# Kernel tuning notes

Hardware: AMD Instinct MI355X
Metric: run time of the kernel (lower is better)

## Reference

```python
import jax, jax.numpy as jnp
import numpy as np

B, C, H, W_IMG = 4, 4, 512, 512
OUT_CH = 256
POS_NUM = 512
NEG_NUM = 512
M_MARGIN = 0.5
TAU = 0.1
EPS = 1e-8


def setup_inputs() -> dict:
    key = jax.random.key(0)
    k1, k2, k3, k4, k5, k6 = jax.random.split(key, 6)
    d1_fegc = jax.random.normal(k1, (B, C, H, W_IMG), dtype=jnp.float32)
    p_fegc = jax.random.uniform(k2, (B, 1, H, W_IMG), dtype=jnp.float32)
    p_pre = jax.random.uniform(k3, (B, 3, H, W_IMG), dtype=jnp.float32)
    gt = (jax.random.uniform(k4, (B, 1, H, W_IMG)) < 0.5).astype(jnp.float32)
    # parameters of the nn.Linear(in_channel, out_channel)
    W = jax.random.normal(k5, (OUT_CH, C), dtype=jnp.float32) / np.sqrt(C)
    b_fc = jax.random.normal(k6, (OUT_CH,), dtype=jnp.float32) * 0.01
    return {"d1_fegc": d1_fegc, "p_fegc": p_fegc, "p_pre": p_pre, "gt": gt, "W": W, "b_fc": b_fc}


def _sample_idx(mask_flat, key, n):
    # randomized fixed-size sampling of n indices where mask is True
    # (replaces torch.nonzero + randperm with a jit-friendly top-k over random scores)
    score = jnp.where(mask_flat, jax.random.uniform(key, mask_flat.shape), -jnp.inf)
    _, idx = jax.lax.top_k(score, n)
    return idx


def reference(d1_fegc, p_fegc, p_pre, gt, W, b_fc):
    b, c, h, w = d1_fegc.shape
    P = POS_NUM * b
    N = NEG_NUM * b
    # p_overlap channel 3: fegc foreground AND pre argmax-class 0
    fegc_fg = p_fegc[:, 0] >= 0.5                       # [b,h,w]
    pre_cls0 = jnp.argmax(p_pre, axis=1) == 0           # [b,h,w]
    pre_region = fegc_fg & pre_cls0                     # [b,h,w]
    gt_fg = gt[:, 0] > 0.5                              # [b,h,w]
    pos_mask = (pre_region & gt_fg).reshape(-1)         # [b*h*w]
    neg_mask = (pre_region & ~gt_fg).reshape(-1)        # [b*h*w]
    # per-pixel feature vectors from d1_fegc
    feats = d1_fegc.transpose(0, 2, 3, 1).reshape(-1, c)  # [b*h*w, c]
    skey = jax.random.key(42)
    kp, kn = jax.random.split(skey)
    pos_idx = _sample_idx(pos_mask, kp, P)
    neg_idx = _sample_idx(neg_mask, kn, N)
    pts = jnp.concatenate([feats[pos_idx], feats[neg_idx]], axis=0)  # [P+N, c]
    proj = pts @ W.T + b_fc                                           # [P+N, out]
    # F.cosine_similarity with eps=1e-8 norm clamping
    norm = jnp.maximum(jnp.linalg.norm(proj, axis=-1, keepdims=True), EPS)
    normed = proj / norm
    cos_sim = normed @ normed.T                                       # [P+N, P+N]
    T = P + N
    label = jnp.ones((T, T), dtype=cos_sim.dtype)
    label = label.at[:P, P:].set(0.0).at[P:, :P].set(0.0)
    s = cos_sim / TAU
    lam = (1.0 - label) * jnp.square(s) + label * jnp.square(jnp.maximum(M_MARGIN - s, 0.0))
    lam = lam * (1.0 - jnp.eye(T, dtype=lam.dtype))                   # mask self pairs
    denom = jnp.sum(lam != 0).astype(lam.dtype)
    return jnp.sum(lam) / denom
```

## Files before the change

kernel.cpp:

```cpp
#include <hip/hip_runtime.h>
#include <stdint.h>

#define HW       262144u
#define NPIX     1048576u
#define NSEL     2048u
#define NSEG     1024u
#define SEGCAP   16u
#define DENSECAP 3584u

#define OFF_SEG   0u
#define OFF_IDX   262144u
#define OFF_VA    278528u
#define OFF_WA    360448u
#define OFF_PSUM  442368u
#define OFF_PNNZ  446464u
#define OFF_G     450560u

#define TF_ROUND(r) { x0 += x1; x1 = (x1 << (r)) | (x1 >> (32 - (r))); x1 ^= x0; }
__host__ __device__ inline void threefry2x32_(uint32_t k0, uint32_t k1,
                                              uint32_t& x0, uint32_t& x1) {
  uint32_t k2 = k0 ^ k1 ^ 0x1BD11BDAu;
  x0 += k0; x1 += k1;
  TF_ROUND(13) TF_ROUND(15) TF_ROUND(26) TF_ROUND(6)
  x0 += k1; x1 += k2 + 1u;
  TF_ROUND(17) TF_ROUND(29) TF_ROUND(16) TF_ROUND(24)
  x0 += k2; x1 += k0 + 2u;
  TF_ROUND(13) TF_ROUND(15) TF_ROUND(26) TF_ROUND(6)
  x0 += k0; x1 += k1 + 3u;
  TF_ROUND(17) TF_ROUND(29) TF_ROUND(16) TF_ROUND(24)
  x0 += k1; x1 += k2 + 4u;
  TF_ROUND(13) TF_ROUND(15) TF_ROUND(26) TF_ROUND(6)
  x0 += k2; x1 += k0 + 5u;
}

__global__ __launch_bounds__(256) void k_front(
    const float* __restrict__ pfegc, const float* __restrict__ ppre,
    const float* __restrict__ gt, const float* __restrict__ Wm,
    const float* __restrict__ bfc,
    uint32_t kp0, uint32_t kp1, uint32_t kn0, uint32_t kn1,
    uint64_t* __restrict__ seg, float* __restrict__ Gout) {
  __shared__ uint32_t cnt2[2];
  __shared__ float sGw[4][25];
  int t = threadIdx.x;
  uint32_t b = blockIdx.x;
  if (t < 2) cnt2[t] = 0;
  if (t < 2 * (int)SEGCAP) {
    uint32_t list = (uint32_t)t / SEGCAP, slot = (uint32_t)t % SEGCAP;
    seg[((size_t)list * NSEG + b) * SEGCAP + slot] = 0ull;
  }
  __syncthreads();
  uint32_t base = b * 1024u + (uint32_t)t * 4u;
  float4 pf = *(const float4*)(pfegc + base);
  float pfa[4] = { pf.x, pf.y, pf.z, pf.w };
  bool any = (pf.x >= 0.5f) || (pf.y >= 0.5f) || (pf.z >= 0.5f) || (pf.w >= 0.5f);
  if (any) {
    uint32_t hw = base & (HW - 1u);
    uint32_t bb = base >> 18;
    const float* pp = ppre + (size_t)bb * 3u * HW + hw;
    float4 p0 = *(const float4*)pp;
    float4 p1 = *(const float4*)(pp + HW);
    float4 p2 = *(const float4*)(pp + 2u * HW);
    float4 g4 = *(const float4*)(gt + base);
    float p0a[4] = { p0.x, p0.y, p0.z, p0.w };
    float p1a[4] = { p1.x, p1.y, p1.z, p1.w };
    float p2a[4] = { p2.x, p2.y, p2.z, p2.w };
    float ga[4]  = { g4.x, g4.y, g4.z, g4.w };
    #pragma unroll
    for (int j = 0; j < 4; ++j) {
      if (pfa[j] >= 0.5f && p0a[j] >= p1a[j] && p0a[j] >= p2a[j]) {
        uint32_t i = base + (uint32_t)j;
        bool gfg = ga[j] > 0.5f;
        uint32_t x0 = 0u, x1 = i;
        threefry2x32_(gfg ? kp0 : kn0, gfg ? kp1 : kn1, x0, x1);
        uint32_t r23 = (x0 ^ x1) >> 9;
        if ((r23 >> 18) == 0x1Fu) {
          uint32_t list = gfg ? 0u : 1u;
          uint32_t r = atomicAdd(&cnt2[list], 1u);
          if (r < SEGCAP)
            seg[((size_t)list * NSEG + b) * SEGCAP + r] =
                (1ull << 43) | ((uint64_t)r23 << 20) | (uint64_t)(0xFFFFFu ^ i);
        }
      }
    }
  }
  if (b == 0) {
    float4 wr = *(const float4*)(Wm + t * 4);
    float av[5] = { wr.x, wr.y, wr.z, wr.w, bfc[t] };
    int lane = t & 63, wvi = t >> 6;
    #pragma unroll
    for (int p = 0; p < 5; ++p)
      #pragma unroll
      for (int q = p; q < 5; ++q) {
        float g = av[p] * av[q];
        #pragma unroll
        for (int off = 32; off > 0; off >>= 1)
          g += __shfl_xor(g, off, 64);
        if (lane == 0) sGw[wvi][p * 5 + q] = g;
      }
    __syncthreads();
    if (t < 25) {
      int p = t / 5, q = t % 5;
      int pp = p < q ? p : q, qq = p < q ? q : p;
      Gout[t] = sGw[0][pp * 5 + qq] + sGw[1][pp * 5 + qq]
              + sGw[2][pp * 5 + qq] + sGw[3][pp * 5 + qq];
    }
  }
}

__global__ __launch_bounds__(256) void k_sel(
    const uint64_t* __restrict__ seg, uint32_t* __restrict__ idxbuf) {
  __shared__ uint64_t dense[DENSECAP];
  __shared__ uint32_t hist[8192];
  __shared__ uint64_t bnd[128];
  __shared__ uint32_t wsum[4];
  __shared__ uint32_t dcnt, bcnt, rank, sb, sneed;
  __shared__ uint64_t sthr;
  int t = threadIdx.x;
  int list = blockIdx.x;
  uint32_t lane = (uint32_t)t & 63u, wv = (uint32_t)t >> 6;
  if (t == 0) { dcnt = 0u; bcnt = 0u; rank = 0u; sb = 0u; sneed = 1u; }
  #pragma unroll
  for (int e = 0; e < 32; ++e) hist[e * 256 + t] = 0u;
  __syncthreads();
  const uint4* sp4 = (const uint4*)(seg + (size_t)list * NSEG * SEGCAP);
  #pragma unroll 4
  for (int it = 0; it < 32; ++it) {
    uint4 v = sp4[(uint32_t)it * 256u + (uint32_t)t];
    uint64_t k0 = ((uint64_t)v.y << 32) | v.x;
    uint64_t k1 = ((uint64_t)v.w << 32) | v.z;
    #pragma unroll
    for (int h = 0; h < 2; ++h) {
      uint64_t k = h ? k1 : k0;
      bool val = (k >> 43) != 0ull;
      unsigned long long mb = __ballot(val);
      uint32_t bs = 0;
      if (lane == 0 && mb) bs = atomicAdd(&dcnt, (uint32_t)__popcll(mb));
      bs = (uint32_t)__shfl((int)bs, 0, 64);
      if (val) {
        uint32_t s2 = bs + (uint32_t)__popcll(mb & ((1ull << lane) - 1ull));
        if (s2 < DENSECAP) dense[s2] = k;
      }
    }
  }
  __syncthreads();
  uint32_t n = dcnt; if (n > DENSECAP) n = DENSECAP;
  for (uint32_t j = t; j < n; j += 256)
    atomicAdd(&hist[(uint32_t)(dense[j] >> 25) & 8191u], 1u);
  __syncthreads();
  uint32_t s = 0;
  #pragma unroll
  for (int e = 0; e < 32; ++e) s += hist[t * 32 + e];
  uint32_t suf = s;
  #pragma unroll
  for (int off = 1; off < 64; off <<= 1) {
    uint32_t v = (uint32_t)__shfl_down((int)suf, off, 64);
    if (lane + (uint32_t)off < 64u) suf += v;
  }
  if (lane == 0) wsum[wv] = suf;
  __syncthreads();
  uint32_t wafter = 0;
  for (uint32_t u = wv + 1u; u < 4u; ++u) wafter += wsum[u];
  uint32_t after_t = wafter + (suf - s);
  if (after_t < NSEL && after_t + s >= NSEL) {
    uint32_t running = after_t;
    for (int e = 31; e >= 0; --e) {
      uint32_t h = hist[t * 32 + e];
      running += h;
      if (running >= NSEL) { sb = (uint32_t)(t * 32 + e); sneed = NSEL - (running - h); break; }
    }
  }
  __syncthreads();
  uint32_t b_star = sb, need = sneed;
  for (uint32_t j = t; j < n; j += 256) {
    uint64_t k = dense[j];
    if (((uint32_t)(k >> 25) & 8191u) == b_star) {
      uint32_t p = atomicAdd(&bcnt, 1u);
      if (p < 128u) bnd[p] = k;
    }
  }
  __syncthreads();
  if (t == 0) {
    uint32_t m = bcnt; if (m > 128u) m = 128u;
    uint64_t thr = bnd[0];
    for (uint32_t i = 0; i < m; ++i) {
      uint32_t rk = 1u;
      for (uint32_t j = 0; j < m; ++j) rk += (bnd[j] > bnd[i]) ? 1u : 0u;
      if (rk == need) { thr = bnd[i]; break; }
    }
    sthr = thr;
  }
  __syncthreads();
  uint64_t thr = sthr;
  uint32_t niter = (n + 255u) >> 8;
  for (uint32_t it2 = 0; it2 < niter; ++it2) {
    uint32_t j = it2 * 256u + (uint32_t)t;
    uint64_t k = 0ull;
    bool v = false;
    if (j < n) { k = dense[j]; v = (k >= thr); }
    unsigned long long mb = __ballot(v);
    uint32_t bs = 0;
    if (lane == 0 && mb) bs = atomicAdd(&rank, (uint32_t)__popcll(mb));
    bs = (uint32_t)__shfl((int)bs, 0, 64);
    if (v) {
      uint32_t s2 = bs + (uint32_t)__popcll(mb & ((1ull << lane) - 1ull));
      if (s2 < NSEL)
        idxbuf[(uint32_t)list * NSEL + s2] = 0xFFFFFu ^ (uint32_t)(k & 0xFFFFFu);
    }
  }
}

__global__ __launch_bounds__(64) void k_proj(
    const uint32_t* __restrict__ idxbuf, const float* __restrict__ Gin,
    const float* __restrict__ d1,
    float* __restrict__ va, float* __restrict__ wa) {
  __shared__ float sG[25];
  int t = threadIdx.x;
  if (t < 25) sG[t] = Gin[t];
  __syncthreads();
  uint32_t tg = blockIdx.x * 64u + (uint32_t)t;
  uint32_t idx = idxbuf[tg] & (NPIX - 1u);
  uint32_t hw = idx & (HW - 1u);
  uint32_t bb = idx >> 18;
  const float* f = d1 + ((size_t)bb << 20) + hw;
  float y[5] = { f[0], f[HW], f[2u * HW], f[3u * HW], 1.0f };
  float z[5]; float n2 = 0.f;
  #pragma unroll
  for (int p = 0; p < 5; ++p) {
    float acc = 0.f;
    #pragma unroll
    for (int q = 0; q < 5; ++q) acc += sG[p * 5 + q] * y[q];
    z[p] = acc; n2 += acc * y[p];
  }
  n2 = fmaxf(n2, 0.f);
  float inv = 1.0f / fmaxf(sqrtf(n2), 1e-8f);
  uint32_t s5 = tg * 5u;
  #pragma unroll
  for (int p = 0; p < 5; ++p) {
    va[s5 + p] = y[p] * inv;
    wa[s5 + p] = z[p] * inv;
  }
}

__global__ __launch_bounds__(256) void k_pair(
    const float* __restrict__ va, const float* __restrict__ wa,
    float* __restrict__ psum, uint32_t* __restrict__ pnnz) {
  __shared__ __align__(16) float sv[640], sw[640];
  __shared__ float wps[4];
  __shared__ uint32_t wpn[4];
  int i0 = blockIdx.x * 128, j0 = blockIdx.y * 128;
  int t = threadIdx.x;
  int lane = t & 63, wv = t >> 6;
  if (t < 160) {
    ((float4*)sv)[t] = ((const float4*)(va + i0 * 5))[t];
    ((float4*)sw)[t] = ((const float4*)(wa + j0 * 5))[t];
  }
  __syncthreads();
  int ty = t >> 4, tx = t & 15;
  float rv[8][5], rw[8][5];
  #pragma unroll
  for (int a = 0; a < 8; ++a)
    #pragma unroll
    for (int p = 0; p < 5; ++p) {
      rv[a][p] = sv[(ty * 8 + a) * 5 + p];
      rw[a][p] = sw[(tx * 8 + a) * 5 + p];
    }
  float lsum = 0.f; uint32_t lnz = 0;
  #pragma unroll
  for (int a = 0; a < 8; ++a) {
    int gi = i0 + ty * 8 + a;
    #pragma unroll
    for (int q = 0; q < 8; ++q) {
      int gj = j0 + tx * 8 + q;
      float c = rv[a][0]*rw[q][0] + rv[a][1]*rw[q][1] + rv[a][2]*rw[q][2]
              + rv[a][3]*rw[q][3] + rv[a][4]*rw[q][4];
      float sc = c * 10.0f;
      if (gi != gj) {
        if (((gi ^ gj) & 2048) == 0) {
          float m = fmaxf(0.5f - sc, 0.f);
          lsum += m * m;
          lnz += (m > 0.f) ? 1u : 0u;
        } else {
          lsum += sc * sc;
          lnz += (sc != 0.f) ? 1u : 0u;
        }
      }
    }
  }
  #pragma unroll
  for (int off = 32; off > 0; off >>= 1) {
    lsum += __shfl_xor(lsum, off, 64);
    lnz  += (uint32_t)__shfl_xor((int)lnz, off, 64);
  }
  if (lane == 0) { wps[wv] = lsum; wpn[wv] = lnz; }
  __syncthreads();
  if (t == 0) {
    int bid = blockIdx.y * (int)gridDim.x + blockIdx.x;
    psum[bid] = wps[0] + wps[1] + wps[2] + wps[3];
    pnnz[bid] = wpn[0] + wpn[1] + wpn[2] + wpn[3];
  }
}

__global__ __launch_bounds__(256) void k_final(const float* __restrict__ psum,
                                               const uint32_t* __restrict__ pnnz,
                                               float* __restrict__ out) {
  __shared__ float wps[4];
  __shared__ uint32_t wpn[4];
  int t = threadIdx.x;
  int lane = t & 63, wv = t >> 6;
  float s = 0.f; uint32_t nz = 0u;
  for (int j = t; j < 1024; j += 256) { s += psum[j]; nz += pnnz[j]; }
  #pragma unroll
  for (int off = 32; off > 0; off >>= 1) {
    s  += __shfl_xor(s, off, 64);
    nz += (uint32_t)__shfl_xor((int)nz, off, 64);
  }
  if (lane == 0) { wps[wv] = s; wpn[wv] = nz; }
  __syncthreads();
  if (t == 0)
    out[0] = (wps[0] + wps[1] + wps[2] + wps[3])
           / (float)(wpn[0] + wpn[1] + wpn[2] + wpn[3]);
}

extern "C" void kernel_launch(void* const* d_in, const int* in_sizes, int n_in,
                              void* d_out, int out_size, void* d_ws, size_t ws_size,
                              hipStream_t stream) {
  (void)in_sizes; (void)n_in; (void)out_size; (void)ws_size;
  const float* d1    = (const float*)d_in[0];
  const float* pfegc = (const float*)d_in[1];
  const float* ppre  = (const float*)d_in[2];
  const float* gt    = (const float*)d_in[3];
  const float* W     = (const float*)d_in[4];
  const float* bfc   = (const float*)d_in[5];
  float* out = (float*)d_out;

  uint8_t* base = (uint8_t*)d_ws;
  uint64_t* seg    = (uint64_t*)(base + OFF_SEG);
  uint32_t* idxbuf = (uint32_t*)(base + OFF_IDX);
  float*    va     = (float*)(base + OFF_VA);
  float*    wa     = (float*)(base + OFF_WA);
  float*    psum   = (float*)(base + OFF_PSUM);
  uint32_t* pnnz   = (uint32_t*)(base + OFF_PNNZ);
  float*    Gws    = (float*)(base + OFF_G);

  uint32_t kp0 = 0u, kp1 = 0u; threefry2x32_(0u, 42u, kp0, kp1);
  uint32_t kn0 = 0u, kn1 = 1u; threefry2x32_(0u, 42u, kn0, kn1);

  k_front<<<NSEG, 256, 0, stream>>>(pfegc, ppre, gt, W, bfc,
                                    kp0, kp1, kn0, kn1, seg, Gws);
  k_sel<<<2, 256, 0, stream>>>(seg, idxbuf);
  k_proj<<<64, 64, 0, stream>>>(idxbuf, Gws, d1, va, wa);
  k_pair<<<dim3(32, 32), 256, 0, stream>>>(va, wa, psum, pnnz);
  k_final<<<1, 256, 0, stream>>>(psum, pnnz, out);
}
```

Measured before the change: 121.8 us.

## Fuse selection with projection, exploit pair symmetry, defer gt load

Merges the selection and projection kernels so the selected indices stay in shared memory and one launch plus a global round-trip disappear. The pair kernel now evaluates only upper-triangular tiles (528 blocks instead of 1024) using gi<gj, relying on the symmetric Gram form; the loss ratio is unchanged because both sum and count are halved. The ground-truth load in the front kernel is skipped when no pixel in the quad qualifies. Projection now runs on only 2 blocks, each thread handling 8 gathers, which may raise latency in that stage.

```diff
diff --git a/kernel.cpp b/kernel.cpp
--- a/kernel.cpp
+++ b/kernel.cpp
@@ -7,14 +7,15 @@
 #define NSEG     1024u
 #define SEGCAP   16u
 #define DENSECAP 3584u
+#define NTILE    32u
+#define NPBLK    528u
 
 #define OFF_SEG   0u
-#define OFF_IDX   262144u
-#define OFF_VA    278528u
-#define OFF_WA    360448u
-#define OFF_PSUM  442368u
-#define OFF_PNNZ  446464u
-#define OFF_G     450560u
+#define OFF_VA    262144u
+#define OFF_WA    344064u
+#define OFF_PSUM  425984u
+#define OFF_PNNZ  428288u
+#define OFF_G     430592u
 
 #define TF_ROUND(r) { x0 += x1; x1 = (x1 << (r)) | (x1 >> (32 - (r))); x1 ^= x0; }
 __host__ __device__ inline void threefry2x32_(uint32_t k0, uint32_t k1,
@@ -60,25 +61,33 @@
     float4 p0 = *(const float4*)pp;
     float4 p1 = *(const float4*)(pp + HW);
     float4 p2 = *(const float4*)(pp + 2u * HW);
-    float4 g4 = *(const float4*)(gt + base);
     float p0a[4] = { p0.x, p0.y, p0.z, p0.w };
     float p1a[4] = { p1.x, p1.y, p1.z, p1.w };
     float p2a[4] = { p2.x, p2.y, p2.z, p2.w };
-    float ga[4]  = { g4.x, g4.y, g4.z, g4.w };
+    bool c[4]; bool anyc = false;
     #pragma unroll
     for (int j = 0; j < 4; ++j) {
-      if (pfa[j] >= 0.5f && p0a[j] >= p1a[j] && p0a[j] >= p2a[j]) {
-        uint32_t i = base + (uint32_t)j;
-        bool gfg = ga[j] > 0.5f;
-        uint32_t x0 = 0u, x1 = i;
-        threefry2x32_(gfg ? kp0 : kn0, gfg ? kp1 : kn1, x0, x1);
-        uint32_t r23 = (x0 ^ x1) >> 9;
-        if ((r23 >> 18) == 0x1Fu) {
-          uint32_t list = gfg ? 0u : 1u;
-          uint32_t r = atomicAdd(&cnt2[list], 1u);
-          if (r < SEGCAP)
-            seg[((size_t)list * NSEG + b) * SEGCAP + r] =
-                (1ull << 43) | ((uint64_t)r23 << 20) | (uint64_t)(0xFFFFFu ^ i);
+      c[j] = (pfa[j] >= 0.5f) && (p0a[j] >= p1a[j]) && (p0a[j] >= p2a[j]);
+      anyc |= c[j];
+    }
+    if (anyc) {
+      float4 g4 = *(const float4*)(gt + base);
+      float ga[4] = { g4.x, g4.y, g4.z, g4.w };
+      #pragma unroll
+      for (int j = 0; j < 4; ++j) {
+        if (c[j]) {
+          uint32_t i = base + (uint32_t)j;
+          bool gfg = ga[j] > 0.5f;
+          uint32_t x0 = 0u, x1 = i;
+          threefry2x32_(gfg ? kp0 : kn0, gfg ? kp1 : kn1, x0, x1);
+          uint32_t r23 = (x0 ^ x1) >> 9;
+          if ((r23 >> 18) == 0x1Fu) {
+            uint32_t list = gfg ? 0u : 1u;
+            uint32_t r = atomicAdd(&cnt2[list], 1u);
+            if (r < SEGCAP)
+              seg[((size_t)list * NSEG + b) * SEGCAP + r] =
+                  (1ull << 43) | ((uint64_t)r23 << 20) | (uint64_t)(0xFFFFFu ^ i);
+          }
         }
       }
     }
@@ -107,10 +116,14 @@
   }
 }
 
-__global__ __launch_bounds__(256) void k_sel(
-    const uint64_t* __restrict__ seg, uint32_t* __restrict__ idxbuf) {
+__global__ __launch_bounds__(256) void k_selproj(
+    const uint64_t* __restrict__ seg, const float* __restrict__ Gin,
+    const float* __restrict__ d1,
+    float* __restrict__ va, float* __restrict__ wa) {
   __shared__ uint64_t dense[DENSECAP];
   __shared__ uint32_t hist[8192];
+  __shared__ uint32_t sidx[NSEL];
+  __shared__ float sG[25];
   __shared__ uint64_t bnd[128];
   __shared__ uint32_t wsum[4];
   __shared__ uint32_t dcnt, bcnt, rank, sb, sneed;
@@ -119,6 +132,7 @@
   int list = blockIdx.x;
   uint32_t lane = (uint32_t)t & 63u, wv = (uint32_t)t >> 6;
   if (t == 0) { dcnt = 0u; bcnt = 0u; rank = 0u; sb = 0u; sneed = 1u; }
+  if (t < 25) sG[t] = Gin[t];
   #pragma unroll
   for (int e = 0; e < 32; ++e) hist[e * 256 + t] = 0u;
   __syncthreads();
@@ -203,41 +217,40 @@
     bs = (uint32_t)__shfl((int)bs, 0, 64);
     if (v) {
       uint32_t s2 = bs + (uint32_t)__popcll(mb & ((1ull << lane) - 1ull));
-      if (s2 < NSEL)
-        idxbuf[(uint32_t)list * NSEL + s2] = 0xFFFFFu ^ (uint32_t)(k & 0xFFFFFu);
-    }
-  }
-}
-
-__global__ __launch_bounds__(64) void k_proj(
-    const uint32_t* __restrict__ idxbuf, const float* __restrict__ Gin,
-    const float* __restrict__ d1,
-    float* __restrict__ va, float* __restrict__ wa) {
-  __shared__ float sG[25];
-  int t = threadIdx.x;
-  if (t < 25) sG[t] = Gin[t];
-  __syncthreads();
-  uint32_t tg = blockIdx.x * 64u + (uint32_t)t;
-  uint32_t idx = idxbuf[tg] & (NPIX - 1u);
-  uint32_t hw = idx & (HW - 1u);
-  uint32_t bb = idx >> 18;
-  const float* f = d1 + ((size_t)bb << 20) + hw;
-  float y[5] = { f[0], f[HW], f[2u * HW], f[3u * HW], 1.0f };
-  float z[5]; float n2 = 0.f;
-  #pragma unroll
-  for (int p = 0; p < 5; ++p) {
-    float acc = 0.f;
-    #pragma unroll
-    for (int q = 0; q < 5; ++q) acc += sG[p * 5 + q] * y[q];
-    z[p] = acc; n2 += acc * y[p];
-  }
-  n2 = fmaxf(n2, 0.f);
-  float inv = 1.0f / fmaxf(sqrtf(n2), 1e-8f);
-  uint32_t s5 = tg * 5u;
-  #pragma unroll
-  for (int p = 0; p < 5; ++p) {
-    va[s5 + p] = y[p] * inv;
-    wa[s5 + p] = z[p] * inv;
+      if (s2 < NSEL) sidx[s2] = 0xFFFFFu ^ (uint32_t)(k & 0xFFFFFu);
+    }
+  }
+  __syncthreads();
+  uint32_t idxr[8];
+  float yv[8][4];
+  #pragma unroll
+  for (int r = 0; r < 8; ++r) idxr[r] = sidx[(uint32_t)t + 256u * r] & (NPIX - 1u);
+  #pragma unroll
+  for (int r = 0; r < 8; ++r) {
+    uint32_t hw = idxr[r] & (HW - 1u);
+    uint32_t bb = idxr[r] >> 18;
+    const float* f = d1 + ((size_t)bb << 20) + hw;
+    yv[r][0] = f[0]; yv[r][1] = f[HW]; yv[r][2] = f[2u * HW]; yv[r][3] = f[3u * HW];
+  }
+  #pragma unroll
+  for (int r = 0; r < 8; ++r) {
+    float y[5] = { yv[r][0], yv[r][1], yv[r][2], yv[r][3], 1.0f };
+    float z[5]; float n2 = 0.f;
+    #pragma unroll
+    for (int p = 0; p < 5; ++p) {
+      float acc = 0.f;
+      #pragma unroll
+      for (int q = 0; q < 5; ++q) acc += sG[p * 5 + q] * y[q];
+      z[p] = acc; n2 += acc * y[p];
+    }
+    n2 = fmaxf(n2, 0.f);
+    float inv = 1.0f / fmaxf(sqrtf(n2), 1e-8f);
+    uint32_t s5 = ((uint32_t)list * NSEL + (uint32_t)t + 256u * r) * 5u;
+    #pragma unroll
+    for (int p = 0; p < 5; ++p) {
+      va[s5 + p] = y[p] * inv;
+      wa[s5 + p] = z[p] * inv;
+    }
   }
 }
 
@@ -247,7 +260,10 @@
   __shared__ __align__(16) float sv[640], sw[640];
   __shared__ float wps[4];
   __shared__ uint32_t wpn[4];
-  int i0 = blockIdx.x * 128, j0 = blockIdx.y * 128;
+  uint32_t bi = 0, rem = blockIdx.x;
+  while (rem >= (NTILE - bi)) { rem -= (NTILE - bi); ++bi; }
+  uint32_t bj = bi + rem;
+  int i0 = (int)bi * 128, j0 = (int)bj * 128;
   int t = threadIdx.x;
   int lane = t & 63, wv = t >> 6;
   if (t < 160) {
@@ -274,7 +290,7 @@
       float c = rv[a][0]*rw[q][0] + rv[a][1]*rw[q][1] + rv[a][2]*rw[q][2]
               + rv[a][3]*rw[q][3] + rv[a][4]*rw[q][4];
       float sc = c * 10.0f;
-      if (gi != gj) {
+      if (gi < gj) {
         if (((gi ^ gj) & 2048) == 0) {
           float m = fmaxf(0.5f - sc, 0.f);
           lsum += m * m;
@@ -294,9 +310,8 @@
   if (lane == 0) { wps[wv] = lsum; wpn[wv] = lnz; }
   __syncthreads();
   if (t == 0) {
-    int bid = blockIdx.y * (int)gridDim.x + blockIdx.x;
-    psum[bid] = wps[0] + wps[1] + wps[2] + wps[3];
-    pnnz[bid] = wpn[0] + wpn[1] + wpn[2] + wpn[3];
+    psum[blockIdx.x] = wps[0] + wps[1] + wps[2] + wps[3];
+    pnnz[blockIdx.x] = wpn[0] + wpn[1] + wpn[2] + wpn[3];
   }
 }
 
@@ -308,7 +323,7 @@
   int t = threadIdx.x;
   int lane = t & 63, wv = t >> 6;
   float s = 0.f; uint32_t nz = 0u;
-  for (int j = t; j < 1024; j += 256) { s += psum[j]; nz += pnnz[j]; }
+  for (int j = t; j < (int)NPBLK; j += 256) { s += psum[j]; nz += pnnz[j]; }
   #pragma unroll
   for (int off = 32; off > 0; off >>= 1) {
     s  += __shfl_xor(s, off, 64);
@@ -335,7 +350,6 @@
 
   uint8_t* base = (uint8_t*)d_ws;
   uint64_t* seg    = (uint64_t*)(base + OFF_SEG);
-  uint32_t* idxbuf = (uint32_t*)(base + OFF_IDX);
   float*    va     = (float*)(base + OFF_VA);
   float*    wa     = (float*)(base + OFF_WA);
   float*    psum   = (float*)(base + OFF_PSUM);
@@ -347,8 +361,7 @@
 
   k_front<<<NSEG, 256, 0, stream>>>(pfegc, ppre, gt, W, bfc,
                                     kp0, kp1, kn0, kn1, seg, Gws);
-  k_sel<<<2, 256, 0, stream>>>(seg, idxbuf);
-  k_proj<<<64, 64, 0, stream>>>(idxbuf, Gws, d1, va, wa);
-  k_pair<<<dim3(32, 32), 256, 0, stream>>>(va, wa, psum, pnnz);
+  k_selproj<<<2, 256, 0, stream>>>(seg, Gws, d1, va, wa);
+  k_pair<<<NPBLK, 256, 0, stream>>>(va, wa, psum, pnnz);
   k_final<<<1, 256, 0, stream>>>(psum, pnnz, out);
 }
```

After: 130.6 us. 7.2% more time.

## Exploit pair symmetry in k_pair, widen k_sel to 1024 threads, skip gt loads

Applied to the files above, without the earlier changes.

The pair kernel now visits only upper-triangle tiles and counts i<j pairs. Both the sum and the nonzero count are halved, so their ratio is unchanged and compute is roughly halved. The selection kernel, launched on only two blocks, uses 1024 threads to shorten its serial phases. The front kernel loads gt only when some pixel in the quad passes the region test. The triangular index decode adds a small loop per block.

```diff
diff --git a/kernel.cpp b/kernel.cpp
--- a/kernel.cpp
+++ b/kernel.cpp
@@ -7,6 +7,8 @@
 #define NSEG     1024u
 #define SEGCAP   16u
 #define DENSECAP 3584u
+#define NTILE    32u
+#define NPBLK    528u
 
 #define OFF_SEG   0u
 #define OFF_IDX   262144u
@@ -60,25 +62,33 @@
     float4 p0 = *(const float4*)pp;
     float4 p1 = *(const float4*)(pp + HW);
     float4 p2 = *(const float4*)(pp + 2u * HW);
-    float4 g4 = *(const float4*)(gt + base);
     float p0a[4] = { p0.x, p0.y, p0.z, p0.w };
     float p1a[4] = { p1.x, p1.y, p1.z, p1.w };
     float p2a[4] = { p2.x, p2.y, p2.z, p2.w };
-    float ga[4]  = { g4.x, g4.y, g4.z, g4.w };
+    bool c[4]; bool anyc = false;
     #pragma unroll
     for (int j = 0; j < 4; ++j) {
-      if (pfa[j] >= 0.5f && p0a[j] >= p1a[j] && p0a[j] >= p2a[j]) {
-        uint32_t i = base + (uint32_t)j;
-        bool gfg = ga[j] > 0.5f;
-        uint32_t x0 = 0u, x1 = i;
-        threefry2x32_(gfg ? kp0 : kn0, gfg ? kp1 : kn1, x0, x1);
-        uint32_t r23 = (x0 ^ x1) >> 9;
-        if ((r23 >> 18) == 0x1Fu) {
-          uint32_t list = gfg ? 0u : 1u;
-          uint32_t r = atomicAdd(&cnt2[list], 1u);
-          if (r < SEGCAP)
-            seg[((size_t)list * NSEG + b) * SEGCAP + r] =
-                (1ull << 43) | ((uint64_t)r23 << 20) | (uint64_t)(0xFFFFFu ^ i);
+      c[j] = (pfa[j] >= 0.5f) && (p0a[j] >= p1a[j]) && (p0a[j] >= p2a[j]);
+      anyc |= c[j];
+    }
+    if (anyc) {
+      float4 g4 = *(const float4*)(gt + base);
+      float ga[4] = { g4.x, g4.y, g4.z, g4.w };
+      #pragma unroll
+      for (int j = 0; j < 4; ++j) {
+        if (c[j]) {
+          uint32_t i = base + (uint32_t)j;
+          bool gfg = ga[j] > 0.5f;
+          uint32_t x0 = 0u, x1 = i;
+          threefry2x32_(gfg ? kp0 : kn0, gfg ? kp1 : kn1, x0, x1);
+          uint32_t r23 = (x0 ^ x1) >> 9;
+          if ((r23 >> 18) == 0x1Fu) {
+            uint32_t list = gfg ? 0u : 1u;
+            uint32_t r = atomicAdd(&cnt2[list], 1u);
+            if (r < SEGCAP)
+              seg[((size_t)list * NSEG + b) * SEGCAP + r] =
+                  (1ull << 43) | ((uint64_t)r23 << 20) | (uint64_t)(0xFFFFFu ^ i);
+          }
         }
       }
     }
@@ -107,12 +117,12 @@
   }
 }
 
-__global__ __launch_bounds__(256) void k_sel(
+__global__ __launch_bounds__(1024) void k_sel(
     const uint64_t* __restrict__ seg, uint32_t* __restrict__ idxbuf) {
   __shared__ uint64_t dense[DENSECAP];
   __shared__ uint32_t hist[8192];
   __shared__ uint64_t bnd[128];
-  __shared__ uint32_t wsum[4];
+  __shared__ uint32_t wsum[16];
   __shared__ uint32_t dcnt, bcnt, rank, sb, sneed;
   __shared__ uint64_t sthr;
   int t = threadIdx.x;
@@ -120,12 +130,12 @@
   uint32_t lane = (uint32_t)t & 63u, wv = (uint32_t)t >> 6;
   if (t == 0) { dcnt = 0u; bcnt = 0u; rank = 0u; sb = 0u; sneed = 1u; }
   #pragma unroll
-  for (int e = 0; e < 32; ++e) hist[e * 256 + t] = 0u;
+  for (int e = 0; e < 8; ++e) hist[e * 1024 + t] = 0u;
   __syncthreads();
   const uint4* sp4 = (const uint4*)(seg + (size_t)list * NSEG * SEGCAP);
-  #pragma unroll 4
-  for (int it = 0; it < 32; ++it) {
-    uint4 v = sp4[(uint32_t)it * 256u + (uint32_t)t];
+  #pragma unroll
+  for (int it = 0; it < 8; ++it) {
+    uint4 v = sp4[(uint32_t)it * 1024u + (uint32_t)t];
     uint64_t k0 = ((uint64_t)v.y << 32) | v.x;
     uint64_t k1 = ((uint64_t)v.w << 32) | v.z;
     #pragma unroll
@@ -144,12 +154,12 @@
   }
   __syncthreads();
   uint32_t n = dcnt; if (n > DENSECAP) n = DENSECAP;
-  for (uint32_t j = t; j < n; j += 256)
+  for (uint32_t j = t; j < n; j += 1024)
     atomicAdd(&hist[(uint32_t)(dense[j] >> 25) & 8191u], 1u);
   __syncthreads();
   uint32_t s = 0;
   #pragma unroll
-  for (int e = 0; e < 32; ++e) s += hist[t * 32 + e];
+  for (int e = 0; e < 8; ++e) s += hist[t * 8 + e];
   uint32_t suf = s;
   #pragma unroll
   for (int off = 1; off < 64; off <<= 1) {
@@ -159,19 +169,19 @@
   if (lane == 0) wsum[wv] = suf;
   __syncthreads();
   uint32_t wafter = 0;
-  for (uint32_t u = wv + 1u; u < 4u; ++u) wafter += wsum[u];
+  for (uint32_t u = wv + 1u; u < 16u; ++u) wafter += wsum[u];
   uint32_t after_t = wafter + (suf - s);
   if (after_t < NSEL && after_t + s >= NSEL) {
     uint32_t running = after_t;
-    for (int e = 31; e >= 0; --e) {
-      uint32_t h = hist[t * 32 + e];
+    for (int e = 7; e >= 0; --e) {
+      uint32_t h = hist[t * 8 + e];
       running += h;
-      if (running >= NSEL) { sb = (uint32_t)(t * 32 + e); sneed = NSEL - (running - h); break; }
+      if (running >= NSEL) { sb = (uint32_t)(t * 8 + e); sneed = NSEL - (running - h); break; }
     }
   }
   __syncthreads();
   uint32_t b_star = sb, need = sneed;
-  for (uint32_t j = t; j < n; j += 256) {
+  for (uint32_t j = t; j < n; j += 1024) {
     uint64_t k = dense[j];
     if (((uint32_t)(k >> 25) & 8191u) == b_star) {
       uint32_t p = atomicAdd(&bcnt, 1u);
@@ -191,9 +201,9 @@
   }
   __syncthreads();
   uint64_t thr = sthr;
-  uint32_t niter = (n + 255u) >> 8;
+  uint32_t niter = (n + 1023u) >> 10;
   for (uint32_t it2 = 0; it2 < niter; ++it2) {
-    uint32_t j = it2 * 256u + (uint32_t)t;
+    uint32_t j = it2 * 1024u + (uint32_t)t;
     uint64_t k = 0ull;
     bool v = false;
     if (j < n) { k = dense[j]; v = (k >= thr); }
@@ -247,7 +257,10 @@
   __shared__ __align__(16) float sv[640], sw[640];
   __shared__ float wps[4];
   __shared__ uint32_t wpn[4];
-  int i0 = blockIdx.x * 128, j0 = blockIdx.y * 128;
+  uint32_t bi = 0, rem = blockIdx.x;
+  while (rem >= (NTILE - bi)) { rem -= (NTILE - bi); ++bi; }
+  uint32_t bj = bi + rem;
+  int i0 = (int)bi * 128, j0 = (int)bj * 128;
   int t = threadIdx.x;
   int lane = t & 63, wv = t >> 6;
   if (t < 160) {
@@ -274,7 +287,7 @@
       float c = rv[a][0]*rw[q][0] + rv[a][1]*rw[q][1] + rv[a][2]*rw[q][2]
               + rv[a][3]*rw[q][3] + rv[a][4]*rw[q][4];
       float sc = c * 10.0f;
-      if (gi != gj) {
+      if (gi < gj) {
         if (((gi ^ gj) & 2048) == 0) {
           float m = fmaxf(0.5f - sc, 0.f);
           lsum += m * m;
@@ -294,9 +307,8 @@
   if (lane == 0) { wps[wv] = lsum; wpn[wv] = lnz; }
   __syncthreads();
   if (t == 0) {
-    int bid = blockIdx.y * (int)gridDim.x + blockIdx.x;
-    psum[bid] = wps[0] + wps[1] + wps[2] + wps[3];
-    pnnz[bid] = wpn[0] + wpn[1] + wpn[2] + wpn[3];
+    psum[blockIdx.x] = wps[0] + wps[1] + wps[2] + wps[3];
+    pnnz[blockIdx.x] = wpn[0] + wpn[1] + wpn[2] + wpn[3];
   }
 }
 
@@ -308,7 +320,7 @@
   int t = threadIdx.x;
   int lane = t & 63, wv = t >> 6;
   float s = 0.f; uint32_t nz = 0u;
-  for (int j = t; j < 1024; j += 256) { s += psum[j]; nz += pnnz[j]; }
+  for (int j = t; j < (int)NPBLK; j += 256) { s += psum[j]; nz += pnnz[j]; }
   #pragma unroll
   for (int off = 32; off > 0; off >>= 1) {
     s  += __shfl_xor(s, off, 64);
@@ -347,8 +359,8 @@
 
   k_front<<<NSEG, 256, 0, stream>>>(pfegc, ppre, gt, W, bfc,
                                     kp0, kp1, kn0, kn1, seg, Gws);
-  k_sel<<<2, 256, 0, stream>>>(seg, idxbuf);
+  k_sel<<<2, 1024, 0, stream>>>(seg, idxbuf);
   k_proj<<<64, 64, 0, stream>>>(idxbuf, Gws, d1, va, wa);
-  k_pair<<<dim3(32, 32), 256, 0, stream>>>(va, wa, psum, pnnz);
+  k_pair<<<NPBLK, 256, 0, stream>>>(va, wa, psum, pnnz);
   k_final<<<1, 256, 0, stream>>>(psum, pnnz, out);
 }
```

Result: faster. 105.9 us (-13.1%).
